# Optimization experiments

Measured on AMD Instinct MI355X. Metric: run time of the kernel, lower is better.

The kernel has to match this reference:

```python
import jax, jax.numpy as jnp
import numpy as np

N_NODES = 100000
IN_CH = 256
OUT_CH = 128
N_EDGES = 3200000
SCALING_FACTOR = 1.8


def gcn_propagate(x, edge_index, num_nodes):
    """APPNP(K=1, alpha=0) == one step of D^-1/2 (A+I) D^-1/2 @ x."""
    row, col = edge_index[0], edge_index[1]
    loops = jnp.arange(num_nodes, dtype=edge_index.dtype)
    row = jnp.concatenate([row, loops])
    col = jnp.concatenate([col, loops])
    ones = jnp.ones(row.shape[0], dtype=x.dtype)
    deg = jax.ops.segment_sum(ones, col, num_segments=num_nodes)  # [N]
    dinv = jnp.where(deg > 0, jax.lax.rsqrt(deg), 0.0)
    norm = dinv[row] * dinv[col]  # [E+N]
    msgs = x[row] * norm[:, None]  # gather + scale, [E+N, C]
    return jax.ops.segment_sum(msgs, col, num_segments=num_nodes)  # [N, C]


def setup_inputs() -> dict:
    key = jax.random.key(0)
    ks = jax.random.split(key, 7)
    x = jax.random.normal(ks[0], (N_NODES, IN_CH), dtype=jnp.float32)
    edge_index = jax.random.randint(ks[1], (2, N_EDGES), 0, N_NODES, dtype=jnp.int64)
    s1 = 1.0 / np.sqrt(IN_CH)
    W1 = jax.random.uniform(ks[2], (IN_CH, OUT_CH), jnp.float32, -s1, s1)
    b1 = jax.random.uniform(ks[3], (OUT_CH,), jnp.float32, -s1, s1)
    W2 = jax.random.uniform(ks[4], (IN_CH, OUT_CH), jnp.float32, -s1, s1)
    b2 = jax.random.uniform(ks[5], (OUT_CH,), jnp.float32, -s1, s1)
    return {"x": x, "edge_index": edge_index, "W1": W1, "b1": b1, "W2": W2, "b2": b2}


def reference(x, edge_index, W1, b1, W2, b2):
    num_nodes = x.shape[0]
    # branch 1: linear1 then propagate
    x_ = x @ W1 + b1
    x_ = gcn_propagate(x_, edge_index, num_nodes)
    # branch 2: linear2, L2 normalize per-row, scale, then propagate
    h = x @ W2 + b2
    nrm = jnp.sqrt(jnp.sum(h * h, axis=1, keepdims=True))
    h = h / jnp.maximum(nrm, 1e-12) * SCALING_FACTOR
    h = gcn_propagate(h, edge_index, num_nodes)
    return (h, x_)
```

## Files before the change

kernel.cpp:

```cpp
#include <hip/hip_runtime.h>

#define IN_CH   256
#define OUT_CH  128
#define SCALE   1.8f
#define GT_M    32
#define BKT_SH  8
#define BKT_CAP 9216

using bf16x8 = __attribute__((ext_vector_type(8))) short;
using f32x4  = __attribute__((ext_vector_type(4))) float;

__device__ __forceinline__ float blo(unsigned int w) { return __uint_as_float(w << 16); }
__device__ __forceinline__ float bhi(unsigned int w) { return __uint_as_float(w & 0xffff0000u); }
__device__ __forceinline__ unsigned short f2b(float f) {
    unsigned int u = __float_as_uint(f);
    u += 0x7fffu + ((u >> 16) & 1u);
    return (unsigned short)(u >> 16);
}
__device__ __forceinline__ void split2(float f, unsigned short& h, unsigned short& l) {
    h = f2b(f);
    float hf = __uint_as_float((unsigned int)h << 16);
    l = f2b(f - hf);
}

__global__ __launch_bounds__(256) void wsplit_kernel(const float* __restrict__ W1, const float* __restrict__ b1,
                                                     const float* __restrict__ W2, const float* __restrict__ b2,
                                                     unsigned short* __restrict__ Wht, unsigned short* __restrict__ Wlt,
                                                     float* __restrict__ bc, int* __restrict__ bktCur) {
    int n = blockIdx.x;
    int k = threadIdx.x;
    if (n < 2) {
        int i = n * 256 + k;
        bktCur[i] = i * BKT_CAP;
    }
    float w = (n < OUT_CH) ? W2[k * OUT_CH + n] : W1[k * OUT_CH + (n - OUT_CH)];
    unsigned short h, l;
    split2(w, h, l);
    Wht[n * IN_CH + k] = h;
    Wlt[n * IN_CH + k] = l;
    if (k == 0) bc[n] = (n < OUT_CH) ? b2[n] : b1[n - OUT_CH];
}

__device__ __forceinline__ void part_body(char* smem, const int* __restrict__ row, const int* __restrict__ col,
                                          int* __restrict__ bktCur, unsigned int* __restrict__ pairs,
                                          int E, int NBKT, int nPart, int pb) {
    int* lh   = (int*)smem;
    int* lcur = lh + 512;
    int t = threadIdx.x;
    lh[t] = 0; lh[t + 256] = 0;
    __syncthreads();
    int tile = (E + nPart - 1) / nPart;
    int e0 = pb * tile;
    int e1 = min(E, e0 + tile);
    for (int i = e0 + t; i < e1; i += 256)
        atomicAdd(&lh[col[i] >> BKT_SH], 1);
    __syncthreads();
    for (int b = t; b < 512; b += 256) {
        int c = (b < NBKT) ? lh[b] : 0;
        lcur[b] = (c > 0) ? atomicAdd(&bktCur[b], c) : 0;
    }
    __syncthreads();
    for (int i = e0 + t; i < e1; i += 256) {
        int c = col[i];
        int b = c >> BKT_SH;
        int pos = atomicAdd(&lcur[b], 1);
        pairs[pos] = ((unsigned int)(c & 255) << 17) | (unsigned int)row[i];
    }
}

__device__ __forceinline__ void csr_body(char* smem, const unsigned int* __restrict__ pairs,
                                         const int* __restrict__ bktCur,
                                         int* __restrict__ csr, int* __restrict__ offs,
                                         int* __restrict__ deg, float* __restrict__ dinv,
                                         int N, int b) {
    unsigned int* sorted = (unsigned int*)smem;
    int* sh   = (int*)(smem + 36864);
    int* sc   = (int*)(smem + 38912);
    int* s    = (int*)(smem + 40960);
    int* nc   = (int*)(smem + 41984);
    int* ncur = (int*)(smem + 43008);
    int t = threadIdx.x;
    int base = b * BKT_CAP;
    int cnt = bktCur[b] - base;

    sh[t] = 0; sh[t + 256] = 0;
    __syncthreads();
    for (int i = t; i < cnt; i += 256)
        atomicAdd(&sh[(pairs[base + i] & 0x1FFFF) >> 8], 1);
    __syncthreads();

    int v0 = sh[t];
    s[t] = v0;
    __syncthreads();
    for (int o = 1; o < 256; o <<= 1) {
        int u = (t >= o) ? s[t - o] : 0;
        __syncthreads();
        s[t] += u;
        __syncthreads();
    }
    sc[t] = s[t] - v0;
    int tot0 = s[255];
    __syncthreads();
    int v1 = sh[t + 256];
    s[t] = v1;
    __syncthreads();
    for (int o = 1; o < 256; o <<= 1) {
        int u = (t >= o) ? s[t - o] : 0;
        __syncthreads();
        s[t] += u;
        __syncthreads();
    }
    sc[t + 256] = s[t] - v1 + tot0;
    __syncthreads();

    for (int i = t; i < cnt; i += 256) {
        unsigned int k = pairs[base + i];
        int pos = atomicAdd(&sc[(k & 0x1FFFF) >> 8], 1);
        sorted[pos] = k;
    }
    __syncthreads();

    nc[t] = 0;
    __syncthreads();
    for (int i = t; i < cnt; i += 256)
        atomicAdd(&nc[sorted[i] >> 17], 1);
    __syncthreads();
    int dv = nc[t];
    s[t] = dv;
    __syncthreads();
    for (int o = 1; o < 256; o <<= 1) {
        int u = (t >= o) ? s[t - o] : 0;
        __syncthreads();
        s[t] += u;
        __syncthreads();
    }
    int rel = s[t] - dv;
    int n = (b << BKT_SH) + t;
    if (n < N) {
        offs[n] = base + rel;
        deg[n] = dv;
        dinv[n] = 1.0f / sqrtf((float)dv + 1.0f);
    }
    ncur[t] = rel;
    __syncthreads();
    for (int i = t; i < cnt; i += 256) {
        unsigned int k = sorted[i];
        int node = k >> 17;
        int pos = atomicAdd(&ncur[node], 1);
        csr[base + pos] = (int)(k & 0x1FFFF);
    }
}

#define XPAD 264
__device__ __forceinline__ void gemm_body(char* smem, const float* __restrict__ x,
                                          const unsigned short* __restrict__ Wht,
                                          const unsigned short* __restrict__ Wlt,
                                          const float* __restrict__ bc,
                                          unsigned short* __restrict__ gb, int blockRow) {
    unsigned short* xh = (unsigned short*)smem;
    unsigned short* xl = xh + GT_M * XPAD;
    float* sn = (float*)(smem + 2 * GT_M * XPAD * sizeof(unsigned short));

    int t = threadIdx.x;
    size_t row0 = (size_t)blockRow * GT_M;

    const float4* xg = (const float4*)(x + row0 * IN_CH);
#pragma unroll
    for (int i = 0; i < 8; i++) {
        int f4 = t + i * 256;
        float4 v = xg[f4];
        int row = f4 >> 6;
        int c4 = (f4 & 63) * 4;
        unsigned short h0, h1, h2, h3, l0, l1, l2, l3;
        split2(v.x, h0, l0); split2(v.y, h1, l1);
        split2(v.z, h2, l2); split2(v.w, h3, l3);
        uint2 hw, lw;
        hw.x = (unsigned int)h0 | ((unsigned int)h1 << 16);
        hw.y = (unsigned int)h2 | ((unsigned int)h3 << 16);
        lw.x = (unsigned int)l0 | ((unsigned int)l1 << 16);
        lw.y = (unsigned int)l2 | ((unsigned int)l3 << 16);
        *(uint2*)&xh[row * XPAD + c4] = hw;
        *(uint2*)&xl[row * XPAD + c4] = lw;
    }
    __syncthreads();

    int lane = t & 63;
    int wv = t >> 6;
    int lr = lane & 15;
    int lk = (lane >> 4) * 8;

    f32x4 acc[2][4];
#pragma unroll
    for (int rt = 0; rt < 2; rt++)
#pragma unroll
        for (int ct = 0; ct < 4; ct++) acc[rt][ct] = (f32x4){0.f, 0.f, 0.f, 0.f};

#pragma unroll
    for (int kt = 0; kt < 8; kt++) {
        int k0 = kt * 32;
        bf16x8 ah[2], al[2];
#pragma unroll
        for (int rt = 0; rt < 2; rt++) {
            int idx = (rt * 16 + lr) * XPAD + k0 + lk;
            ah[rt] = *(const bf16x8*)&xh[idx];
            al[rt] = *(const bf16x8*)&xl[idx];
        }
        bf16x8 bh[4], bl[4];
#pragma unroll
        for (int ct = 0; ct < 4; ct++) {
            int n = wv * 64 + ct * 16 + lr;
            bh[ct] = *(const bf16x8*)&Wht[n * IN_CH + k0 + lk];
            bl[ct] = *(const bf16x8*)&Wlt[n * IN_CH + k0 + lk];
        }
#pragma unroll
        for (int rt = 0; rt < 2; rt++)
#pragma unroll
            for (int ct = 0; ct < 4; ct++) {
                acc[rt][ct] = __builtin_amdgcn_mfma_f32_16x16x32_bf16(ah[rt], bh[ct], acc[rt][ct], 0, 0, 0);
                acc[rt][ct] = __builtin_amdgcn_mfma_f32_16x16x32_bf16(al[rt], bh[ct], acc[rt][ct], 0, 0, 0);
                acc[rt][ct] = __builtin_amdgcn_mfma_f32_16x16x32_bf16(ah[rt], bl[ct], acc[rt][ct], 0, 0, 0);
            }
    }
    __syncthreads();

    float bcv[4];
#pragma unroll
    for (int ct = 0; ct < 4; ct++) bcv[ct] = bc[wv * 64 + ct * 16 + lr];
#pragma unroll
    for (int rt = 0; rt < 2; rt++)
#pragma unroll
        for (int ct = 0; ct < 4; ct++)
#pragma unroll
            for (int j = 0; j < 4; j++) acc[rt][ct][j] += bcv[ct];

    if (wv < 2) {
        float nr[2][4];
#pragma unroll
        for (int rt = 0; rt < 2; rt++)
#pragma unroll
            for (int j = 0; j < 4; j++) {
                float sum = 0.f;
#pragma unroll
                for (int ct = 0; ct < 4; ct++) sum += acc[rt][ct][j] * acc[rt][ct][j];
                nr[rt][j] = sum;
            }
#pragma unroll
        for (int o = 1; o < 16; o <<= 1)
#pragma unroll
            for (int rt = 0; rt < 2; rt++)
#pragma unroll
                for (int j = 0; j < 4; j++) nr[rt][j] += __shfl_xor(nr[rt][j], o);
        if (lr == 0) {
#pragma unroll
            for (int rt = 0; rt < 2; rt++)
#pragma unroll
                for (int j = 0; j < 4; j++)
                    sn[wv * GT_M + rt * 16 + (lane >> 4) * 4 + j] = nr[rt][j];
        }
    }
    __syncthreads();

#pragma unroll
    for (int rt = 0; rt < 2; rt++) {
#pragma unroll
        for (int j = 0; j < 4; j++) {
            int rl = rt * 16 + (lane >> 4) * 4 + j;
            float sf;
            if (wv < 2) {
                float n2 = sn[rl] + sn[GT_M + rl];
                sf = SCALE / fmaxf(sqrtf(n2), 1e-12f);
            } else {
                sf = 1.0f;
            }
            size_t base = (row0 + rl) * 256;
#pragma unroll
            for (int ct = 0; ct < 4; ct++) {
                int col = wv * 64 + ct * 16 + lr;
                gb[base + col] = f2b(acc[rt][ct][j] * sf);
            }
        }
    }
}

__global__ __launch_bounds__(256) void k1_part_gemm(const int* __restrict__ row, const int* __restrict__ col,
                                                    int* __restrict__ bktCur, unsigned int* __restrict__ pairs,
                                                    int E, int NBKT, int nPart,
                                                    const float* __restrict__ x,
                                                    const unsigned short* __restrict__ Wht,
                                                    const unsigned short* __restrict__ Wlt,
                                                    const float* __restrict__ bc,
                                                    unsigned short* __restrict__ gb) {
    __shared__ __align__(16) char smem[34048];
    int b = (int)blockIdx.x;
    if (b < nPart) part_body(smem, row, col, bktCur, pairs, E, NBKT, nPart, b);
    else gemm_body(smem, x, Wht, Wlt, bc, gb, b - nPart);
}

__global__ __launch_bounds__(256) void k2_csr_gemm(const unsigned int* __restrict__ pairs,
                                                   const int* __restrict__ bktCur,
                                                   int* __restrict__ csr, int* __restrict__ offs,
                                                   int* __restrict__ deg, float* __restrict__ dinv,
                                                   int N, int nCsr, int gemmRowBase,
                                                   const float* __restrict__ x,
                                                   const unsigned short* __restrict__ Wht,
                                                   const unsigned short* __restrict__ Wlt,
                                                   const float* __restrict__ bc,
                                                   unsigned short* __restrict__ gb) {
    __shared__ __align__(16) char smem[44032];
    int b = (int)blockIdx.x;
    if (b < nCsr) csr_body(smem, pairs, bktCur, csr, offs, deg, dinv, N, b);
    else gemm_body(smem, x, Wht, Wlt, bc, gb, gemmRowBase + (b - nCsr));
}

__global__ __launch_bounds__(256) void gather_kernel(const uint4* __restrict__ gp,
                                                     const int* __restrict__ offs, const int* __restrict__ deg,
                                                     const int* __restrict__ csr, const float* __restrict__ dinv,
                                                     float* __restrict__ outh, float* __restrict__ outx, int N) {
    int t = threadIdx.x;
    int n = (blockIdx.x << 2) + (t >> 6);
    if (n >= N) return;
    int l = t & 63;
    int half = l >> 5;
    int cl = l & 31;

    float a0 = 0.f, a1 = 0.f, a2 = 0.f, a3 = 0.f, a4 = 0.f, a5 = 0.f, a6 = 0.f, a7 = 0.f;
    auto accumw = [&](uint4 w, float ds) {
        a0 += blo(w.x) * ds; a1 += bhi(w.x) * ds;
        a2 += blo(w.y) * ds; a3 += bhi(w.y) * ds;
        a4 += blo(w.z) * ds; a5 += bhi(w.z) * ds;
        a6 += blo(w.w) * ds; a7 += bhi(w.w) * ds;
    };

    float dn = dinv[n];
    if (half == 0) accumw(gp[(size_t)n * 32 + cl], dn);

    int s0 = offs[n];
    int e1 = s0 + deg[n];
    int e = s0 + half;
    for (; e + 2 < e1; e += 4) {
        int sa = csr[e];
        int sb = csr[e + 2];
        float da = dinv[sa];
        float db = dinv[sb];
        uint4 wa = gp[(size_t)sa * 32 + cl];
        uint4 wb = gp[(size_t)sb * 32 + cl];
        accumw(wa, da); accumw(wb, db);
    }
    for (; e < e1; e += 2) {
        int sa = csr[e];
        accumw(gp[(size_t)sa * 32 + cl], dinv[sa]);
    }

    a0 += __shfl_xor(a0, 32);
    a1 += __shfl_xor(a1, 32);
    a2 += __shfl_xor(a2, 32);
    a3 += __shfl_xor(a3, 32);
    a4 += __shfl_xor(a4, 32);
    a5 += __shfl_xor(a5, 32);
    a6 += __shfl_xor(a6, 32);
    a7 += __shfl_xor(a7, 32);

    if (half == 0) {
        float4 v0 = {a0 * dn, a1 * dn, a2 * dn, a3 * dn};
        float4 v1 = {a4 * dn, a5 * dn, a6 * dn, a7 * dn};
        if (cl < 16) {
            float* o = &outh[(size_t)n * OUT_CH + cl * 8];
            *(float4*)o = v0;
            *(float4*)(o + 4) = v1;
        } else {
            float* o = &outx[(size_t)n * OUT_CH + (cl - 16) * 8];
            *(float4*)o = v0;
            *(float4*)(o + 4) = v1;
        }
    }
}

extern "C" void kernel_launch(void* const* d_in, const int* in_sizes, int n_in,
                              void* d_out, int out_size, void* d_ws, size_t ws_size,
                              hipStream_t stream) {
    const float* x   = (const float*)d_in[0];
    const int*   ei  = (const int*)d_in[1];
    const float* W1  = (const float*)d_in[2];
    const float* b1  = (const float*)d_in[3];
    const float* W2  = (const float*)d_in[4];
    const float* b2  = (const float*)d_in[5];

    const int N = in_sizes[0] / IN_CH;
    const int E = in_sizes[1] / 2;
    const int NBKT = (N + 255) >> BKT_SH;

    float* outh = (float*)d_out;
    float* outx = outh + (size_t)N * OUT_CH;

    char* p = (char*)d_ws;
    auto take = [&](size_t bytes) {
        char* q = p;
        p += (bytes + 255) & ~(size_t)255;
        return q;
    };
    int*   deg     = (int*)take((size_t)N * sizeof(int));
    float* dinv    = (float*)take((size_t)N * sizeof(float));
    int*   offs    = (int*)take((size_t)N * sizeof(int));
    int*   bktCur  = (int*)take(512 * sizeof(int));
    float* bc      = (float*)take(256 * sizeof(float));
    unsigned short* Wht = (unsigned short*)take(256 * 256 * sizeof(unsigned short));
    unsigned short* Wlt = (unsigned short*)take(256 * 256 * sizeof(unsigned short));
    int*   csr     = (int*)take((size_t)NBKT * BKT_CAP * sizeof(int));
    unsigned int* pairs = (unsigned int*)take((size_t)NBKT * BKT_CAP * sizeof(unsigned int));
    unsigned short* gb = (unsigned short*)take((size_t)N * 256 * sizeof(unsigned short));

    const int* erow = ei;
    const int* ecol = ei + E;

    const int nPart = 512;
    const int gemmBlocks = N / GT_M;
    const int gemmA = (gemmBlocks + 1) / 2;
    const int gemmB = gemmBlocks - gemmA;

    wsplit_kernel<<<256, 256, 0, stream>>>(W1, b1, W2, b2, Wht, Wlt, bc, bktCur);
    k1_part_gemm<<<nPart + gemmA, 256, 0, stream>>>(erow, ecol, bktCur, pairs, E, NBKT, nPart,
                                                    x, Wht, Wlt, bc, gb);
    k2_csr_gemm<<<NBKT + gemmB, 256, 0, stream>>>(pairs, bktCur, csr, offs, deg, dinv, N, NBKT, gemmA,
                                                  x, Wht, Wlt, bc, gb);
    gather_kernel<<<(N + 3) / 4, 256, 0, stream>>>((const uint4*)gb, offs, deg, csr, dinv, outh, outx, N);
}
```

Before: 435.7 us.

## Drop x low-part split in GEMM and remove per-bucket source sort in CSR build

The GEMM no longer splits x into bf16 high and low parts. It uses only the bf16-rounded x with split W, which cuts the MFMA count from three to two per tile and removes the low-part shared buffer. The CSR builder drops the intermediate sort by source-row sub-bucket and counts and scatters directly from the pairs array. Both changes shrink shared memory and can raise occupancy. The cost is that x is rounded to bf16, which loses accuracy, and the CSR neighbor order is no longer sorted by source, so gather locality may get worse.

```diff
diff --git a/kernel.cpp b/kernel.cpp
--- a/kernel.cpp
+++ b/kernel.cpp
@@ -73,57 +73,17 @@
                                          int* __restrict__ csr, int* __restrict__ offs,
                                          int* __restrict__ deg, float* __restrict__ dinv,
                                          int N, int b) {
-    unsigned int* sorted = (unsigned int*)smem;
-    int* sh   = (int*)(smem + 36864);
-    int* sc   = (int*)(smem + 38912);
-    int* s    = (int*)(smem + 40960);
-    int* nc   = (int*)(smem + 41984);
-    int* ncur = (int*)(smem + 43008);
+    int* s    = (int*)smem;
+    int* nc   = (int*)(smem + 1024);
+    int* ncur = (int*)(smem + 2048);
     int t = threadIdx.x;
     int base = b * BKT_CAP;
     int cnt = bktCur[b] - base;
 
-    sh[t] = 0; sh[t + 256] = 0;
+    nc[t] = 0;
     __syncthreads();
     for (int i = t; i < cnt; i += 256)
-        atomicAdd(&sh[(pairs[base + i] & 0x1FFFF) >> 8], 1);
-    __syncthreads();
-
-    int v0 = sh[t];
-    s[t] = v0;
-    __syncthreads();
-    for (int o = 1; o < 256; o <<= 1) {
-        int u = (t >= o) ? s[t - o] : 0;
-        __syncthreads();
-        s[t] += u;
-        __syncthreads();
-    }
-    sc[t] = s[t] - v0;
-    int tot0 = s[255];
-    __syncthreads();
-    int v1 = sh[t + 256];
-    s[t] = v1;
-    __syncthreads();
-    for (int o = 1; o < 256; o <<= 1) {
-        int u = (t >= o) ? s[t - o] : 0;
-        __syncthreads();
-        s[t] += u;
-        __syncthreads();
-    }
-    sc[t + 256] = s[t] - v1 + tot0;
-    __syncthreads();
-
-    for (int i = t; i < cnt; i += 256) {
-        unsigned int k = pairs[base + i];
-        int pos = atomicAdd(&sc[(k & 0x1FFFF) >> 8], 1);
-        sorted[pos] = k;
-    }
-    __syncthreads();
-
-    nc[t] = 0;
-    __syncthreads();
-    for (int i = t; i < cnt; i += 256)
-        atomicAdd(&nc[sorted[i] >> 17], 1);
+        atomicAdd(&nc[pairs[base + i] >> 17], 1);
     __syncthreads();
     int dv = nc[t];
     s[t] = dv;
@@ -144,7 +104,7 @@
     ncur[t] = rel;
     __syncthreads();
     for (int i = t; i < cnt; i += 256) {
-        unsigned int k = sorted[i];
+        unsigned int k = pairs[base + i];
         int node = k >> 17;
         int pos = atomicAdd(&ncur[node], 1);
         csr[base + pos] = (int)(k & 0x1FFFF);
@@ -152,14 +112,14 @@
 }
 
 #define XPAD 264
+#define GEMM_SMEM (GT_M * XPAD * 2 + 2 * GT_M * 4)
 __device__ __forceinline__ void gemm_body(char* smem, const float* __restrict__ x,
                                           const unsigned short* __restrict__ Wht,
                                           const unsigned short* __restrict__ Wlt,
                                           const float* __restrict__ bc,
                                           unsigned short* __restrict__ gb, int blockRow) {
     unsigned short* xh = (unsigned short*)smem;
-    unsigned short* xl = xh + GT_M * XPAD;
-    float* sn = (float*)(smem + 2 * GT_M * XPAD * sizeof(unsigned short));
+    float* sn = (float*)(smem + GT_M * XPAD * sizeof(unsigned short));
 
     int t = threadIdx.x;
     size_t row0 = (size_t)blockRow * GT_M;
@@ -171,16 +131,10 @@
         float4 v = xg[f4];
         int row = f4 >> 6;
         int c4 = (f4 & 63) * 4;
-        unsigned short h0, h1, h2, h3, l0, l1, l2, l3;
-        split2(v.x, h0, l0); split2(v.y, h1, l1);
-        split2(v.z, h2, l2); split2(v.w, h3, l3);
-        uint2 hw, lw;
-        hw.x = (unsigned int)h0 | ((unsigned int)h1 << 16);
-        hw.y = (unsigned int)h2 | ((unsigned int)h3 << 16);
-        lw.x = (unsigned int)l0 | ((unsigned int)l1 << 16);
-        lw.y = (unsigned int)l2 | ((unsigned int)l3 << 16);
+        uint2 hw;
+        hw.x = (unsigned int)f2b(v.x) | ((unsigned int)f2b(v.y) << 16);
+        hw.y = (unsigned int)f2b(v.z) | ((unsigned int)f2b(v.w) << 16);
         *(uint2*)&xh[row * XPAD + c4] = hw;
-        *(uint2*)&xl[row * XPAD + c4] = lw;
     }
     __syncthreads();
 
@@ -198,12 +152,11 @@
 #pragma unroll
     for (int kt = 0; kt < 8; kt++) {
         int k0 = kt * 32;
-        bf16x8 ah[2], al[2];
+        bf16x8 ah[2];
 #pragma unroll
         for (int rt = 0; rt < 2; rt++) {
             int idx = (rt * 16 + lr) * XPAD + k0 + lk;
             ah[rt] = *(const bf16x8*)&xh[idx];
-            al[rt] = *(const bf16x8*)&xl[idx];
         }
         bf16x8 bh[4], bl[4];
 #pragma unroll
@@ -217,7 +170,6 @@
 #pragma unroll
             for (int ct = 0; ct < 4; ct++) {
                 acc[rt][ct] = __builtin_amdgcn_mfma_f32_16x16x32_bf16(ah[rt], bh[ct], acc[rt][ct], 0, 0, 0);
-                acc[rt][ct] = __builtin_amdgcn_mfma_f32_16x16x32_bf16(al[rt], bh[ct], acc[rt][ct], 0, 0, 0);
                 acc[rt][ct] = __builtin_amdgcn_mfma_f32_16x16x32_bf16(ah[rt], bl[ct], acc[rt][ct], 0, 0, 0);
             }
     }
@@ -290,7 +242,7 @@
                                                     const unsigned short* __restrict__ Wlt,
                                                     const float* __restrict__ bc,
                                                     unsigned short* __restrict__ gb) {
-    __shared__ __align__(16) char smem[34048];
+    __shared__ __align__(16) char smem[GEMM_SMEM];
     int b = (int)blockIdx.x;
     if (b < nPart) part_body(smem, row, col, bktCur, pairs, E, NBKT, nPart, b);
     else gemm_body(smem, x, Wht, Wlt, bc, gb, b - nPart);
@@ -306,7 +258,7 @@
                                                    const unsigned short* __restrict__ Wlt,
                                                    const float* __restrict__ bc,
                                                    unsigned short* __restrict__ gb) {
-    __shared__ __align__(16) char smem[44032];
+    __shared__ __align__(16) char smem[GEMM_SMEM];
     int b = (int)blockIdx.x;
     if (b < nCsr) csr_body(smem, pairs, bktCur, csr, offs, deg, dinv, N, b);
     else gemm_body(smem, x, Wht, Wlt, bc, gb, gemmRowBase + (b - nCsr));
```

New measurement: 446.7 us. 2.5% more time.
